# Optimization experiments

Hardware: AMD Instinct MI355X
Metric: run time of the kernel (lower is better)

Reference implementation:

```python
import jax, jax.numpy as jnp
import numpy as np

N_NODES = 50000
N_EDGES = 800000
IN_DIM = 128
HID = 64
HEADS = 4
OUT_DIM = 128
NEG_SLOPE = 0.2


def setup_inputs() -> dict:
    key = jax.random.key(0)
    ks = jax.random.split(key, 11)
    x = jax.random.normal(ks[0], (N_NODES, IN_DIM), dtype=jnp.float32)
    edge_index = jax.random.randint(ks[1], (2, N_EDGES), 0, N_NODES, dtype=jnp.int64)
    s1 = 1.0 / np.sqrt(IN_DIM)
    s2 = 1.0 / np.sqrt(HEADS * HID)
    W1 = jax.random.normal(ks[2], (IN_DIM, HEADS * HID), dtype=jnp.float32) * s1
    a_src1 = jax.random.normal(ks[3], (HEADS, HID), dtype=jnp.float32) * s2
    a_dst1 = jax.random.normal(ks[4], (HEADS, HID), dtype=jnp.float32) * s2
    b1 = jnp.zeros((HEADS * HID,), dtype=jnp.float32)
    W2 = jax.random.normal(ks[5], (HEADS * HID, OUT_DIM), dtype=jnp.float32) * s2
    a_src2 = jax.random.normal(ks[6], (1, OUT_DIM), dtype=jnp.float32) * 0.1
    a_dst2 = jax.random.normal(ks[7], (1, OUT_DIM), dtype=jnp.float32) * 0.1
    b2 = jnp.zeros((OUT_DIM,), dtype=jnp.float32)
    return {"x": x, "edge_index": edge_index, "W1": W1, "a_src1": a_src1,
            "a_dst1": a_dst1, "b1": b1, "W2": W2, "a_src2": a_src2,
            "a_dst2": a_dst2, "b2": b2}


def _gat_conv(x, src, dst, W, a_src, a_dst, bias, heads, out_per_head, concat):
    n = x.shape[0]
    # linear projection per head: [N, H, F]
    h = (x @ W).reshape(n, heads, out_per_head)
    # per-node attention terms: [N, H]
    alpha_src = jnp.einsum('nhf,hf->nh', h, a_src)
    alpha_dst = jnp.einsum('nhf,hf->nh', h, a_dst)
    # edge logits with LeakyReLU: [E, H]
    e = jax.nn.leaky_relu(alpha_src[src] + alpha_dst[dst], NEG_SLOPE)
    # softmax over incoming edges of each destination node
    m = jax.ops.segment_max(e, dst, num_segments=n)  # [N, H]
    m = jnp.where(jnp.isfinite(m), m, 0.0)
    e = jnp.exp(e - m[dst])
    denom = jax.ops.segment_sum(e, dst, num_segments=n)  # [N, H]
    alpha = e / (denom[dst] + 1e-16)  # [E, H]
    # weighted scatter-aggregate of source messages
    out = jax.ops.segment_sum(h[src] * alpha[:, :, None], dst, num_segments=n)  # [N, H, F]
    if concat:
        out = out.reshape(n, heads * out_per_head)
    else:
        out = out.mean(axis=1)
    return out + bias


def reference(x, edge_index, W1, a_src1, a_dst1, b1, W2, a_src2, a_dst2, b2):
    n = x.shape[0]
    # PyG GATConv adds self-loops by default
    loops = jnp.arange(n, dtype=edge_index.dtype)
    src = jnp.concatenate([edge_index[0], loops])
    dst = jnp.concatenate([edge_index[1], loops])
    # dropout layers are identity in inference
    h = _gat_conv(x, src, dst, W1, a_src1, a_dst1, b1, HEADS, HID, True)
    h = jax.nn.elu(h)
    out = _gat_conv(h, src, dst, W2, a_src2, a_dst2, b2, 1, OUT_DIM, True)
    # F.normalize(p=2, dim=1)
    norm = jnp.linalg.norm(out, axis=1, keepdims=True)
    return out / jnp.maximum(norm, 1e-12)
```

## Files before the change

### kernel.cpp

```cpp
#include <hip/hip_runtime.h>
#include <hip/hip_fp16.h>
#include <math.h>

#define N_NODES 50000
#define N_EDGES 800000
#define ET (N_EDGES + N_NODES)
#define IN_DIM 128
#define HID 64
#define HEADS 4
#define C1 (HEADS * HID)
#define OUT_DIM 128
#define NEG_SLOPE 0.2f
#define MTILES 3125
#define SCAN_B 1024
#define NSCB 49
#define HB 64
#define EPB (N_EDGES / HB)

typedef _Float16 h8 __attribute__((ext_vector_type(8)));
typedef float f4 __attribute__((ext_vector_type(4)));
typedef unsigned short u16;

__device__ __forceinline__ float leaky(float v) { return fmaxf(v, NEG_SLOPE * v); }
__device__ __forceinline__ float elu(float v) { return v > 0.0f ? v : expm1f(v); }

__device__ __forceinline__ void fma_mix8(float* acc, h8 v, float w) {
    union { h8 h; int i[4]; } u; u.h = v;
#pragma unroll
    for (int k = 0; k < 4; ++k) {
        asm("v_fma_mix_f32 %0, %1, %2, %0 op_sel:[0,0,0] op_sel_hi:[1,0,0]"
            : "+v"(acc[2 * k]) : "v"(u.i[k]), "v"(w));
        asm("v_fma_mix_f32 %0, %1, %2, %0 op_sel:[1,0,0] op_sel_hi:[1,0,0]"
            : "+v"(acc[2 * k + 1]) : "v"(u.i[k]), "v"(w));
    }
}

__global__ __launch_bounds__(256) void hist_kernel(
        const float* __restrict__ W1, const float* __restrict__ W2,
        const int* __restrict__ dst, __half* __restrict__ w1t,
        __half* __restrict__ w2t, u16* __restrict__ cnt_mat,
        u16* __restrict__ lrank16) {
    __shared__ unsigned pk[N_NODES / 4];
    const int b = blockIdx.x, t = threadIdx.x;
    for (int i = b * 256 + t; i < IN_DIM * C1; i += HB * 256) {
        int k1 = i >> 8, n1 = i & 255;
        w1t[n1 * IN_DIM + k1] = __float2half(W1[i]);
        int k2 = i >> 7, n2 = i & 127;
        w2t[n2 * C1 + k2] = __float2half(W2[i]);
    }
    const int e0 = b * EPB;
#pragma unroll
    for (int half = 0; half < 2; ++half) {
        const int nbase = half * (N_NODES / 2);
        for (int i = t; i < N_NODES / 4; i += 256) pk[i] = 0;
        __syncthreads();
        for (int k = t; k < EPB; k += 256) {
            int d = dst[e0 + k] - nbase;
            if ((unsigned)d < (unsigned)(N_NODES / 2)) {
                unsigned r = atomicAdd(&pk[d >> 1], (d & 1) ? 65536u : 1u);
                lrank16[e0 + k] = (u16)((d & 1) ? (r >> 16) : (r & 0xffffu));
            }
        }
        __syncthreads();
        unsigned* crow = (unsigned*)(cnt_mat + (size_t)b * N_NODES) + half * (N_NODES / 4);
        for (int i = t; i < N_NODES / 4; i += 256) crow[i] = pk[i];
        __syncthreads();
    }
}

__global__ void scan_local(const u16* __restrict__ cnt_mat, u16* __restrict__ boff,
                           int* __restrict__ lscan, int* __restrict__ bsum) {
    __shared__ int wsum[16];
    const int t = threadIdx.x, lane = t & 63, wv = t >> 6;
    int idx = blockIdx.x * SCAN_B + t;
    int run = 0;
    if (idx < N_NODES) {
#pragma unroll 8
        for (int b = 0; b < HB; ++b) {
            u16 c = cnt_mat[(size_t)b * N_NODES + idx];
            boff[(size_t)b * N_NODES + idx] = (u16)run;
            run += c;
        }
    }
    int v = (idx < N_NODES) ? run + 1 : 0;
    int sc = v;
#pragma unroll
    for (int o = 1; o < 64; o <<= 1) {
        int u = __shfl_up(sc, o);
        if (lane >= o) sc += u;
    }
    if (lane == 63) wsum[wv] = sc;
    __syncthreads();
    if (t == 0) {
        int run2 = 0;
#pragma unroll
        for (int w = 0; w < 16; ++w) { int s = wsum[w]; wsum[w] = run2; run2 += s; }
        bsum[blockIdx.x] = run2;
    }
    __syncthreads();
    if (idx < N_NODES) lscan[idx] = sc + wsum[wv];
}

__global__ void scan_bsum(int* __restrict__ bsum) {
    const int t = threadIdx.x;
    int v = (t < NSCB) ? bsum[t] : 0;
    int sc = v;
#pragma unroll
    for (int o = 1; o < 64; o <<= 1) {
        int u = __shfl_up(sc, o);
        if (t >= o) sc += u;
    }
    if (t < NSCB) bsum[t] = sc - v;
}

__global__ void scan_final(const int* __restrict__ lscan, const int* __restrict__ bsum,
                           int* __restrict__ rp) {
    int idx = blockIdx.x * SCAN_B + threadIdx.x;
    if (idx == 0) rp[0] = 0;
    if (idx >= N_NODES) return;
    rp[idx + 1] = lscan[idx] + bsum[idx >> 10];
}

__global__ void scatter_plain(const int* __restrict__ src, const int* __restrict__ dst,
                              const u16* __restrict__ lrank16, const u16* __restrict__ boff,
                              const int* __restrict__ rp, u16* __restrict__ cs16) {
    const int tid = blockIdx.x * blockDim.x + threadIdx.x;
    if (tid < N_EDGES / 4) {
        const int b = tid / (EPB / 4);
        const u16* bo = boff + (size_t)b * N_NODES;
        int4 s4 = ((const int4*)src)[tid];
        int4 d4 = ((const int4*)dst)[tid];
        ushort4 r4 = ((const ushort4*)lrank16)[tid];
        cs16[rp[d4.x] + (int)bo[d4.x] + (int)r4.x] = (u16)s4.x;
        cs16[rp[d4.y] + (int)bo[d4.y] + (int)r4.y] = (u16)s4.y;
        cs16[rp[d4.z] + (int)bo[d4.z] + (int)r4.z] = (u16)s4.z;
        cs16[rp[d4.w] + (int)bo[d4.w] + (int)r4.w] = (u16)s4.w;
    } else {
        int d = tid - N_EDGES / 4;
        if (d < N_NODES) cs16[rp[d + 1] - 1] = (u16)d;
    }
}

__global__ __launch_bounds__(256) void gemm1_mfma(
        const float* __restrict__ x, const __half* __restrict__ w1t,
        const float* __restrict__ aws, const float* __restrict__ awd,
        __half* __restrict__ hpm, float* __restrict__ as1m, float* __restrict__ ad1m) {
    const int tile = blockIdx.x * 4 + (threadIdx.x >> 6);
    if (tile >= MTILES) return;
    const int lane = threadIdx.x & 63;
    const int m0 = tile * 16, lm = lane & 15, lq = lane >> 4;
    h8 afrag[4];
    const float4* xrow = (const float4*)(x + (size_t)(m0 + lm) * IN_DIM + lq * 8);
#pragma unroll
    for (int kt = 0; kt < 4; ++kt) {
        float4 a = xrow[kt * 8];
        float4 b = xrow[kt * 8 + 1];
        union { h8 v; __half2 p[4]; } u;
        u.p[0] = __floats2half2_rn(a.x, a.y);
        u.p[1] = __floats2half2_rn(a.z, a.w);
        u.p[2] = __floats2half2_rn(b.x, b.y);
        u.p[3] = __floats2half2_rn(b.z, b.w);
        afrag[kt] = u.v;
    }
    f4 acc[16];
#pragma unroll
    for (int nt = 0; nt < 16; ++nt) acc[nt] = (f4){0.f, 0.f, 0.f, 0.f};
#pragma unroll
    for (int nt = 0; nt < 16; ++nt) {
        const h8* brow = (const h8*)(w1t + (size_t)(nt * 16 + lm) * IN_DIM + lq * 8);
#pragma unroll
        for (int kt = 0; kt < 4; ++kt)
            acc[nt] = __builtin_amdgcn_mfma_f32_16x16x32_f16(afrag[kt], brow[kt * 4],
                                                             acc[nt], 0, 0, 0);
    }
    float sS[4][4] = {{0.f}}, sD[4][4] = {{0.f}};
#pragma unroll
    for (int nt = 0; nt < 16; ++nt) {
        int col = nt * 16 + lm;
        float wa = aws[col], wd = awd[col];
        int hd = nt >> 2;
        int pr = nt >> 3;
        int cip = col & 127;
#pragma unroll
        for (int r = 0; r < 4; ++r) {
            float v = acc[nt][r];
            hpm[((size_t)pr * N_NODES + (m0 + lq * 4 + r)) * 128 + cip] = __float2half(v);
            sS[hd][r] += v * wa;
            sD[hd][r] += v * wd;
        }
    }
#pragma unroll
    for (int o = 1; o < 16; o <<= 1) {
#pragma unroll
        for (int hd = 0; hd < 4; ++hd)
#pragma unroll
            for (int r = 0; r < 4; ++r) {
                sS[hd][r] += __shfl_xor(sS[hd][r], o);
                sD[hd][r] += __shfl_xor(sD[hd][r], o);
            }
    }
    if (lm == 0) {
        float2* asp = (float2*)as1m;
        float2* adp = (float2*)ad1m;
#pragma unroll
        for (int r = 0; r < 4; ++r) {
            int row = m0 + lq * 4 + r;
            asp[row]           = make_float2(sS[0][r], sS[1][r]);
            asp[N_NODES + row] = make_float2(sS[2][r], sS[3][r]);
            adp[row]           = make_float2(sD[0][r], sD[1][r]);
            adp[N_NODES + row] = make_float2(sD[2][r], sD[3][r]);
        }
    }
}

__global__ __launch_bounds__(256) void gemm2_mfma(
        const __half* __restrict__ ah, const __half* __restrict__ w2t,
        const float* __restrict__ aws, const float* __restrict__ awd,
        __half* __restrict__ h, float* __restrict__ as2, float* __restrict__ ad2) {
    const int tile = blockIdx.x * 4 + (threadIdx.x >> 6);
    if (tile >= MTILES) return;
    const int lane = threadIdx.x & 63;
    const int m0 = tile * 16, lm = lane & 15, lq = lane >> 4;
    h8 afrag[8];
    const h8* arow = (const h8*)(ah + (size_t)(m0 + lm) * C1 + lq * 8);
#pragma unroll
    for (int kt = 0; kt < 8; ++kt) afrag[kt] = arow[kt * 4];
    f4 acc[8];
#pragma unroll
    for (int nt = 0; nt < 8; ++nt) acc[nt] = (f4){0.f, 0.f, 0.f, 0.f};
#pragma unroll
    for (int nt = 0; nt < 8; ++nt) {
        const h8* brow = (const h8*)(w2t + (size_t)(nt * 16 + lm) * C1 + lq * 8);
#pragma unroll
        for (int kt = 0; kt < 8; ++kt)
            acc[nt] = __builtin_amdgcn_mfma_f32_16x16x32_f16(afrag[kt], brow[kt * 4],
                                                             acc[nt], 0, 0, 0);
    }
    float sS[4] = {0.f, 0.f, 0.f, 0.f}, sD[4] = {0.f, 0.f, 0.f, 0.f};
#pragma unroll
    for (int nt = 0; nt < 8; ++nt) {
        int col = nt * 16 + lm;
        float wa = aws[col], wd = awd[col];
#pragma unroll
        for (int r = 0; r < 4; ++r) {
            float v = acc[nt][r];
            h[(size_t)(m0 + lq * 4 + r) * OUT_DIM + col] = __float2half(v);
            sS[r] += v * wa;
            sD[r] += v * wd;
        }
    }
#pragma unroll
    for (int o = 1; o < 16; o <<= 1) {
#pragma unroll
        for (int r = 0; r < 4; ++r) {
            sS[r] += __shfl_xor(sS[r], o);
            sD[r] += __shfl_xor(sD[r], o);
        }
    }
    if (lm == 0) {
#pragma unroll
        for (int r = 0; r < 4; ++r) {
            int row = m0 + lq * 4 + r;
            as2[row] = sS[r];
            ad2[row] = sD[r];
        }
    }
}

__global__ __launch_bounds__(256) void aggregate1_fused(
        const int* __restrict__ rp, const u16* __restrict__ cs16,
        const __half* __restrict__ hpm, const float* __restrict__ as1m,
        const float* __restrict__ ad1m, const float* __restrict__ b1,
        __half* __restrict__ out1h) {
    __shared__ int4 stg[8][32];
    const int pair = blockIdx.x & 1, g = blockIdx.x >> 1;
    const int hw = threadIdx.x >> 5, li = threadIdx.x & 31;
    const int d = g * 8 + hw;
    const int e0 = rp[d], deg = rp[d + 1] - e0;
    const float2* asb = (const float2*)as1m + (size_t)pair * N_NODES;
    const float2 adv = ((const float2*)ad1m)[(size_t)pair * N_NODES + d];
    const char* hb = (const char*)hpm + (size_t)pair * N_NODES * 256;
    const int es = li >> 4, fl = li & 15;
    const int hip = fl >> 3;
    const int lbyte = fl * 16;
    float acc[8] = {0.f, 0.f, 0.f, 0.f, 0.f, 0.f, 0.f, 0.f};
    float ds0 = 0.f, ds1 = 0.f;
    for (int c0 = 0; c0 < deg; c0 += 32) {
        const int clen = min(32, deg - c0);
        int idx = c0 + li;
        bool valid = idx < deg;
        int s = valid ? (int)cs16[e0 + idx] : 0;
        float2 av = asb[s];
        float x0 = valid ? __expf(leaky(av.x + adv.x)) : 0.f;
        float x1 = valid ? __expf(leaky(av.y + adv.y)) : 0.f;
        stg[hw][li] = make_int4(s << 8, __float_as_int(x0), __float_as_int(x1), 0);
        ds0 += x0; ds1 += x1;
        __builtin_amdgcn_wave_barrier();
        int j = 0;
        for (; j + 8 <= clen; j += 8) {
            int4 p0 = stg[hw][j + es];
            int4 p1 = stg[hw][j + 2 + es];
            int4 p2 = stg[hw][j + 4 + es];
            int4 p3 = stg[hw][j + 6 + es];
            h8 v0 = *(const h8*)(hb + p0.x + lbyte);
            h8 v1 = *(const h8*)(hb + p1.x + lbyte);
            h8 v2 = *(const h8*)(hb + p2.x + lbyte);
            h8 v3 = *(const h8*)(hb + p3.x + lbyte);
            fma_mix8(acc, v0, __int_as_float(hip ? p0.z : p0.y));
            fma_mix8(acc, v1, __int_as_float(hip ? p1.z : p1.y));
            fma_mix8(acc, v2, __int_as_float(hip ? p2.z : p2.y));
            fma_mix8(acc, v3, __int_as_float(hip ? p3.z : p3.y));
        }
        for (; j < clen; j += 2) {
            int4 p0 = stg[hw][j + es];
            h8 v0 = *(const h8*)(hb + p0.x + lbyte);
            fma_mix8(acc, v0, __int_as_float(hip ? p0.z : p0.y));
        }
        __builtin_amdgcn_wave_barrier();
    }
#pragma unroll
    for (int f = 0; f < 8; ++f) acc[f] += __shfl_xor(acc[f], 16);
#pragma unroll
    for (int o = 16; o > 0; o >>= 1) {
        ds0 += __shfl_xor(ds0, o);
        ds1 += __shfl_xor(ds1, o);
    }
    if (es == 0) {
        float den = hip ? ds1 : ds0;
        float inv = 1.0f / (den + 1e-16f);
        float4 bA = ((const float4*)b1)[pair * 32 + fl * 2];
        float4 bB = ((const float4*)b1)[pair * 32 + fl * 2 + 1];
        h8 o;
        o[0] = (_Float16)elu(acc[0] * inv + bA.x);
        o[1] = (_Float16)elu(acc[1] * inv + bA.y);
        o[2] = (_Float16)elu(acc[2] * inv + bA.z);
        o[3] = (_Float16)elu(acc[3] * inv + bA.w);
        o[4] = (_Float16)elu(acc[4] * inv + bB.x);
        o[5] = (_Float16)elu(acc[5] * inv + bB.y);
        o[6] = (_Float16)elu(acc[6] * inv + bB.z);
        o[7] = (_Float16)elu(acc[7] * inv + bB.w);
        *(h8*)((char*)out1h + (size_t)d * 512 + pair * 256 + lbyte) = o;
    }
}

__global__ __launch_bounds__(256) void aggregate2_fused(
        const int* __restrict__ rp, const u16* __restrict__ cs16,
        const __half* __restrict__ h2h, const float* __restrict__ as2,
        const float* __restrict__ ad2, const float* __restrict__ b2,
        float* __restrict__ out) {
    __shared__ int2 stg[8][32];
    const int hw = threadIdx.x >> 5, li = threadIdx.x & 31;
    const int d = blockIdx.x * 8 + hw;
    const int e0 = rp[d], deg = rp[d + 1] - e0;
    const float adv = ad2[d];
    const int q = li >> 4, lo = li & 15;
    const int lbyte = lo * 16;
    const char* hbase = (const char*)h2h;
    float acc[8] = {0.f, 0.f, 0.f, 0.f, 0.f, 0.f, 0.f, 0.f};
    float dsum = 0.f;
    for (int c0 = 0; c0 < deg; c0 += 32) {
        const int clen = min(32, deg - c0);
        int idx = c0 + li;
        bool valid = idx < deg;
        int s = valid ? (int)cs16[e0 + idx] : 0;
        float xv = valid ? __expf(leaky(as2[s] + adv)) : 0.f;
        stg[hw][li] = make_int2(s << 8, __float_as_int(xv));
        dsum += xv;
        __builtin_amdgcn_wave_barrier();
        int j = 0;
        for (; j + 8 <= clen; j += 8) {
            int2 p0 = stg[hw][j + q];
            int2 p1 = stg[hw][j + 2 + q];
            int2 p2 = stg[hw][j + 4 + q];
            int2 p3 = stg[hw][j + 6 + q];
            h8 v0 = *(const h8*)(hbase + p0.x + lbyte);
            h8 v1 = *(const h8*)(hbase + p1.x + lbyte);
            h8 v2 = *(const h8*)(hbase + p2.x + lbyte);
            h8 v3 = *(const h8*)(hbase + p3.x + lbyte);
            fma_mix8(acc, v0, __int_as_float(p0.y));
            fma_mix8(acc, v1, __int_as_float(p1.y));
            fma_mix8(acc, v2, __int_as_float(p2.y));
            fma_mix8(acc, v3, __int_as_float(p3.y));
        }
        for (; j < clen; j += 2) {
            int2 p0 = stg[hw][j + q];
            h8 v0 = *(const h8*)(hbase + p0.x + lbyte);
            fma_mix8(acc, v0, __int_as_float(p0.y));
        }
        __builtin_amdgcn_wave_barrier();
    }
#pragma unroll
    for (int f = 0; f < 8; ++f) acc[f] += __shfl_xor(acc[f], 16);
#pragma unroll
    for (int o = 16; o > 0; o >>= 1) dsum += __shfl_xor(dsum, o);
    if (q == 0) {
        float inv = 1.0f / (dsum + 1e-16f);
        float4 bA = ((const float4*)b2)[lo * 2];
        float4 bB = ((const float4*)b2)[lo * 2 + 1];
        float v0 = acc[0] * inv + bA.x, v1 = acc[1] * inv + bA.y;
        float v2 = acc[2] * inv + bA.z, v3 = acc[3] * inv + bA.w;
        float v4 = acc[4] * inv + bB.x, v5 = acc[5] * inv + bB.y;
        float v6 = acc[6] * inv + bB.z, v7 = acc[7] * inv + bB.w;
        float ss = v0 * v0 + v1 * v1 + v2 * v2 + v3 * v3 +
                   v4 * v4 + v5 * v5 + v6 * v6 + v7 * v7;
#pragma unroll
        for (int o = 1; o < 16; o <<= 1) ss += __shfl_xor(ss, o);
        float sc = 1.0f / fmaxf(sqrtf(ss), 1e-12f);
        float4* orow = (float4*)((char*)out + (size_t)d * 512 + lo * 32);
        orow[0] = make_float4(v0 * sc, v1 * sc, v2 * sc, v3 * sc);
        orow[1] = make_float4(v4 * sc, v5 * sc, v6 * sc, v7 * sc);
    }
}

extern "C" void kernel_launch(void* const* d_in, const int* in_sizes, int n_in,
                              void* d_out, int out_size, void* d_ws, size_t ws_size,
                              hipStream_t stream) {
    const float* x     = (const float*)d_in[0];
    const int*   edge  = (const int*)d_in[1];
    const int*   src   = edge;
    const int*   dst   = edge + N_EDGES;
    const float* W1    = (const float*)d_in[2];
    const float* aw_s1 = (const float*)d_in[3];
    const float* aw_d1 = (const float*)d_in[4];
    const float* b1    = (const float*)d_in[5];
    const float* W2    = (const float*)d_in[6];
    const float* aw_s2 = (const float*)d_in[7];
    const float* aw_d2 = (const float*)d_in[8];
    const float* b2    = (const float*)d_in[9];
    float* out = (float*)d_out;

    char* ws = (char*)d_ws;
    size_t off = 0;
    auto alloc = [&](size_t bytes) {
        void* p = ws + off;
        off += (bytes + 255) & ~(size_t)255;
        return p;
    };
    u16*    cs16    = (u16*)alloc((size_t)ET * 2);
    u16*    lrank16 = (u16*)alloc((size_t)N_EDGES * 2);
    u16*    cnt_mat = (u16*)alloc((size_t)HB * N_NODES * 2);
    u16*    boff    = (u16*)alloc((size_t)HB * N_NODES * 2);
    int*    rp      = (int*)alloc((size_t)(N_NODES + 1) * 4);
    int*    lscan   = (int*)alloc((size_t)NSCB * SCAN_B * 4);
    int*    bsum    = (int*)alloc((size_t)NSCB * 4);
    float*  as1     = (float*)alloc((size_t)N_NODES * HEADS * 4);
    float*  ad1     = (float*)alloc((size_t)N_NODES * HEADS * 4);
    float*  as2     = (float*)alloc((size_t)N_NODES * 4);
    float*  ad2     = (float*)alloc((size_t)N_NODES * 4);
    __half* w1t     = (__half*)alloc((size_t)IN_DIM * C1 * 2);
    __half* w2t     = (__half*)alloc((size_t)C1 * OUT_DIM * 2);
    __half* hpm     = (__half*)alloc((size_t)N_NODES * C1 * 2);
    __half* out1h   = (__half*)alloc((size_t)N_NODES * C1 * 2);
    __half* h2h     = hpm;
    (void)off;


    hist_kernel<<<HB, 256, 0, stream>>>(W1, W2, dst, w1t, w2t, cnt_mat, lrank16);
    scan_local<<<NSCB, SCAN_B, 0, stream>>>(cnt_mat, boff, lscan, bsum);
    scan_bsum<<<1, 64, 0, stream>>>(bsum);
    scan_final<<<NSCB, SCAN_B, 0, stream>>>(lscan, bsum, rp);
    scatter_plain<<<(N_EDGES / 4 + N_NODES + 255) / 256, 256, 0, stream>>>(
        src, dst, lrank16, boff, rp, cs16);

    gemm1_mfma<<<(MTILES + 3) / 4, 256, 0, stream>>>(x, w1t, aw_s1, aw_d1, hpm, as1, ad1);
    aggregate1_fused<<<(N_NODES / 8) * 2, 256, 0, stream>>>(rp, cs16, hpm, as1, ad1, b1, out1h);

    gemm2_mfma<<<(MTILES + 3) / 4, 256, 0, stream>>>(out1h, w2t, aw_s2, aw_d2, h2h, as2, ad2);
    aggregate2_fused<<<N_NODES / 8, 256, 0, stream>>>(rp, cs16, h2h, as2, ad2, b2, out);
}
```

Measured before the change: 312.2 us.

## Fuse destination histogram into gemm1 launch and fold block-sum scan into final scan

```diff
diff --git a/kernel.cpp b/kernel.cpp
--- a/kernel.cpp
+++ b/kernel.cpp
@@ -12,10 +12,13 @@
 #define OUT_DIM 128
 #define NEG_SLOPE 0.2f
 #define MTILES 3125
+#define G1GRP 782
 #define SCAN_B 1024
 #define NSCB 49
 #define HB 64
 #define EPB (N_EDGES / HB)
+#define HQ 4
+#define NQN (N_NODES / HQ)
 
 typedef _Float16 h8 __attribute__((ext_vector_type(8)));
 typedef float f4 __attribute__((ext_vector_type(4)));
@@ -35,36 +38,109 @@
     }
 }
 
-__global__ __launch_bounds__(256) void hist_kernel(
-        const float* __restrict__ W1, const float* __restrict__ W2,
-        const int* __restrict__ dst, __half* __restrict__ w1t,
-        __half* __restrict__ w2t, u16* __restrict__ cnt_mat,
+__global__ void transpose_w(const float* __restrict__ W1, const float* __restrict__ W2,
+                            __half* __restrict__ w1t, __half* __restrict__ w2t) {
+    int i = blockIdx.x * 256 + threadIdx.x;
+    int k1 = i >> 8, n1 = i & 255;
+    w1t[n1 * IN_DIM + k1] = __float2half(W1[i]);
+    int k2 = i >> 7, n2 = i & 127;
+    w2t[n2 * C1 + k2] = __float2half(W2[i]);
+}
+
+__global__ __launch_bounds__(256) void gemm1_hist(
+        const float* __restrict__ x, const __half* __restrict__ w1t,
+        const float* __restrict__ aws, const float* __restrict__ awd,
+        __half* __restrict__ hpm, float* __restrict__ as1m, float* __restrict__ ad1m,
+        const int* __restrict__ dst, u16* __restrict__ cnt_mat,
         u16* __restrict__ lrank16) {
-    __shared__ unsigned pk[N_NODES / 4];
-    const int b = blockIdx.x, t = threadIdx.x;
-    for (int i = b * 256 + t; i < IN_DIM * C1; i += HB * 256) {
-        int k1 = i >> 8, n1 = i & 255;
-        w1t[n1 * IN_DIM + k1] = __float2half(W1[i]);
-        int k2 = i >> 7, n2 = i & 127;
-        w2t[n2 * C1 + k2] = __float2half(W2[i]);
-    }
-    const int e0 = b * EPB;
-#pragma unroll
-    for (int half = 0; half < 2; ++half) {
-        const int nbase = half * (N_NODES / 2);
-        for (int i = t; i < N_NODES / 4; i += 256) pk[i] = 0;
-        __syncthreads();
-        for (int k = t; k < EPB; k += 256) {
-            int d = dst[e0 + k] - nbase;
-            if ((unsigned)d < (unsigned)(N_NODES / 2)) {
-                unsigned r = atomicAdd(&pk[d >> 1], (d & 1) ? 65536u : 1u);
-                lrank16[e0 + k] = (u16)((d & 1) ? (r >> 16) : (r & 0xffffu));
+    __shared__ unsigned pk[NQN / 2];
+    if (blockIdx.x < HB) {
+        const int b = blockIdx.x, t = threadIdx.x;
+        const int e0 = b * EPB;
+#pragma unroll
+        for (int qd = 0; qd < HQ; ++qd) {
+            const int nbase = qd * NQN;
+            for (int i = t; i < NQN / 2; i += 256) pk[i] = 0;
+            __syncthreads();
+            for (int k = t; k < EPB; k += 256) {
+                int d = dst[e0 + k] - nbase;
+                if ((unsigned)d < (unsigned)NQN) {
+                    unsigned r = atomicAdd(&pk[d >> 1], (d & 1) ? 65536u : 1u);
+                    lrank16[e0 + k] = (u16)((d & 1) ? (r >> 16) : (r & 0xffffu));
+                }
             }
-        }
-        __syncthreads();
-        unsigned* crow = (unsigned*)(cnt_mat + (size_t)b * N_NODES) + half * (N_NODES / 4);
-        for (int i = t; i < N_NODES / 4; i += 256) crow[i] = pk[i];
-        __syncthreads();
+            __syncthreads();
+            unsigned* crow = (unsigned*)(cnt_mat + (size_t)b * N_NODES) + qd * (NQN / 2);
+            for (int i = t; i < NQN / 2; i += 256) crow[i] = pk[i];
+            __syncthreads();
+        }
+        return;
+    }
+    const int tile = (blockIdx.x - HB) * 4 + (threadIdx.x >> 6);
+    if (tile >= MTILES) return;
+    const int lane = threadIdx.x & 63;
+    const int m0 = tile * 16, lm = lane & 15, lq = lane >> 4;
+    h8 afrag[4];
+    const float4* xrow = (const float4*)(x + (size_t)(m0 + lm) * IN_DIM + lq * 8);
+#pragma unroll
+    for (int kt = 0; kt < 4; ++kt) {
+        float4 a = xrow[kt * 8];
+        float4 b = xrow[kt * 8 + 1];
+        union { h8 v; __half2 p[4]; } u;
+        u.p[0] = __floats2half2_rn(a.x, a.y);
+        u.p[1] = __floats2half2_rn(a.z, a.w);
+        u.p[2] = __floats2half2_rn(b.x, b.y);
+        u.p[3] = __floats2half2_rn(b.z, b.w);
+        afrag[kt] = u.v;
+    }
+    f4 acc[16];
+#pragma unroll
+    for (int nt = 0; nt < 16; ++nt) acc[nt] = (f4){0.f, 0.f, 0.f, 0.f};
+#pragma unroll
+    for (int nt = 0; nt < 16; ++nt) {
+        const h8* brow = (const h8*)(w1t + (size_t)(nt * 16 + lm) * IN_DIM + lq * 8);
+#pragma unroll
+        for (int kt = 0; kt < 4; ++kt)
+            acc[nt] = __builtin_amdgcn_mfma_f32_16x16x32_f16(afrag[kt], brow[kt * 4],
+                                                             acc[nt], 0, 0, 0);
+    }
+    float sS[4][4] = {{0.f}}, sD[4][4] = {{0.f}};
+#pragma unroll
+    for (int nt = 0; nt < 16; ++nt) {
+        int col = nt * 16 + lm;
+        float wa = aws[col], wd = awd[col];
+        int hd = nt >> 2;
+        int pr = nt >> 3;
+        int cip = col & 127;
+#pragma unroll
+        for (int r = 0; r < 4; ++r) {
+            float v = acc[nt][r];
+            hpm[((size_t)pr * N_NODES + (m0 + lq * 4 + r)) * 128 + cip] = __float2half(v);
+            sS[hd][r] += v * wa;
+            sD[hd][r] += v * wd;
+        }
+    }
+#pragma unroll
+    for (int o = 1; o < 16; o <<= 1) {
+#pragma unroll
+        for (int hd = 0; hd < 4; ++hd)
+#pragma unroll
+            for (int r = 0; r < 4; ++r) {
+                sS[hd][r] += __shfl_xor(sS[hd][r], o);
+                sD[hd][r] += __shfl_xor(sD[hd][r], o);
+            }
+    }
+    if (lm == 0) {
+        float2* asp = (float2*)as1m;
+        float2* adp = (float2*)ad1m;
+#pragma unroll
+        for (int r = 0; r < 4; ++r) {
+            int row = m0 + lq * 4 + r;
+            asp[row]           = make_float2(sS[0][r], sS[1][r]);
+            asp[N_NODES + row] = make_float2(sS[2][r], sS[3][r]);
+            adp[row]           = make_float2(sD[0][r], sD[1][r]);
+            adp[N_NODES + row] = make_float2(sD[2][r], sD[3][r]);
+        }
     }
 }
 
@@ -101,24 +177,19 @@
     if (idx < N_NODES) lscan[idx] = sc + wsum[wv];
 }
 
-__global__ void scan_bsum(int* __restrict__ bsum) {
-    const int t = threadIdx.x;
-    int v = (t < NSCB) ? bsum[t] : 0;
-    int sc = v;
-#pragma unroll
-    for (int o = 1; o < 64; o <<= 1) {
-        int u = __shfl_up(sc, o);
-        if (t >= o) sc += u;
-    }
-    if (t < NSCB) bsum[t] = sc - v;
-}
-
 __global__ void scan_final(const int* __restrict__ lscan, const int* __restrict__ bsum,
                            int* __restrict__ rp) {
+    __shared__ int base;
+    if (threadIdx.x == 0) {
+        int s = 0;
+        for (int b = 0; b < blockIdx.x; ++b) s += bsum[b];
+        base = s;
+    }
+    __syncthreads();
     int idx = blockIdx.x * SCAN_B + threadIdx.x;
     if (idx == 0) rp[0] = 0;
     if (idx >= N_NODES) return;
-    rp[idx + 1] = lscan[idx] + bsum[idx >> 10];
+    rp[idx + 1] = lscan[idx] + base;
 }
 
 __global__ void scatter_plain(const int* __restrict__ src, const int* __restrict__ dst,
@@ -138,78 +209,6 @@
     } else {
         int d = tid - N_EDGES / 4;
         if (d < N_NODES) cs16[rp[d + 1] - 1] = (u16)d;
-    }
-}
-
-__global__ __launch_bounds__(256) void gemm1_mfma(
-        const float* __restrict__ x, const __half* __restrict__ w1t,
-        const float* __restrict__ aws, const float* __restrict__ awd,
-        __half* __restrict__ hpm, float* __restrict__ as1m, float* __restrict__ ad1m) {
-    const int tile = blockIdx.x * 4 + (threadIdx.x >> 6);
-    if (tile >= MTILES) return;
-    const int lane = threadIdx.x & 63;
-    const int m0 = tile * 16, lm = lane & 15, lq = lane >> 4;
-    h8 afrag[4];
-    const float4* xrow = (const float4*)(x + (size_t)(m0 + lm) * IN_DIM + lq * 8);
-#pragma unroll
-    for (int kt = 0; kt < 4; ++kt) {
-        float4 a = xrow[kt * 8];
-        float4 b = xrow[kt * 8 + 1];
-        union { h8 v; __half2 p[4]; } u;
-        u.p[0] = __floats2half2_rn(a.x, a.y);
-        u.p[1] = __floats2half2_rn(a.z, a.w);
-        u.p[2] = __floats2half2_rn(b.x, b.y);
-        u.p[3] = __floats2half2_rn(b.z, b.w);
-        afrag[kt] = u.v;
-    }
-    f4 acc[16];
-#pragma unroll
-    for (int nt = 0; nt < 16; ++nt) acc[nt] = (f4){0.f, 0.f, 0.f, 0.f};
-#pragma unroll
-    for (int nt = 0; nt < 16; ++nt) {
-        const h8* brow = (const h8*)(w1t + (size_t)(nt * 16 + lm) * IN_DIM + lq * 8);
-#pragma unroll
-        for (int kt = 0; kt < 4; ++kt)
-            acc[nt] = __builtin_amdgcn_mfma_f32_16x16x32_f16(afrag[kt], brow[kt * 4],
-                                                             acc[nt], 0, 0, 0);
-    }
-    float sS[4][4] = {{0.f}}, sD[4][4] = {{0.f}};
-#pragma unroll
-    for (int nt = 0; nt < 16; ++nt) {
-        int col = nt * 16 + lm;
-        float wa = aws[col], wd = awd[col];
-        int hd = nt >> 2;
-        int pr = nt >> 3;
-        int cip = col & 127;
-#pragma unroll
-        for (int r = 0; r < 4; ++r) {
-            float v = acc[nt][r];
-            hpm[((size_t)pr * N_NODES + (m0 + lq * 4 + r)) * 128 + cip] = __float2half(v);
-            sS[hd][r] += v * wa;
-            sD[hd][r] += v * wd;
-        }
-    }
-#pragma unroll
-    for (int o = 1; o < 16; o <<= 1) {
-#pragma unroll
-        for (int hd = 0; hd < 4; ++hd)
-#pragma unroll
-            for (int r = 0; r < 4; ++r) {
-                sS[hd][r] += __shfl_xor(sS[hd][r], o);
-                sD[hd][r] += __shfl_xor(sD[hd][r], o);
-            }
-    }
-    if (lm == 0) {
-        float2* asp = (float2*)as1m;
-        float2* adp = (float2*)ad1m;
-#pragma unroll
-        for (int r = 0; r < 4; ++r) {
-            int row = m0 + lq * 4 + r;
-            asp[row]           = make_float2(sS[0][r], sS[1][r]);
-            asp[N_NODES + row] = make_float2(sS[2][r], sS[3][r]);
-            adp[row]           = make_float2(sD[0][r], sD[1][r]);
-            adp[N_NODES + row] = make_float2(sD[2][r], sD[3][r]);
-        }
     }
 }
 
@@ -455,14 +454,16 @@
     (void)off;
 
 
-    hist_kernel<<<HB, 256, 0, stream>>>(W1, W2, dst, w1t, w2t, cnt_mat, lrank16);
+    transpose_w<<<(IN_DIM * C1) / 256, 256, 0, stream>>>(W1, W2, w1t, w2t);
+
+    gemm1_hist<<<HB + G1GRP, 256, 0, stream>>>(x, w1t, aw_s1, aw_d1, hpm, as1, ad1,
+                                               dst, cnt_mat, lrank16);
+
     scan_local<<<NSCB, SCAN_B, 0, stream>>>(cnt_mat, boff, lscan, bsum);
-    scan_bsum<<<1, 64, 0, stream>>>(bsum);
     scan_final<<<NSCB, SCAN_B, 0, stream>>>(lscan, bsum, rp);
     scatter_plain<<<(N_EDGES / 4 + N_NODES + 255) / 256, 256, 0, stream>>>(
         src, dst, lrank16, boff, rp, cs16);
 
-    gemm1_mfma<<<(MTILES + 3) / 4, 256, 0, stream>>>(x, w1t, aw_s1, aw_d1, hpm, as1, ad1);
     aggregate1_fused<<<(N_NODES / 8) * 2, 256, 0, stream>>>(rp, cs16, hpm, as1, ad1, b1, out1h);
 
     gemm2_mfma<<<(MTILES + 3) / 4, 256, 0, stream>>>(out1h, w2t, aw_s2, aw_d2, h2h, as2, ad2);
```

After: 306.3 us. Within noise of the previous version (-1.9%).
